# Performance work log

Hardware: AMD Instinct MI355X
Metric: run time of the kernel (lower is better)

## Reference

```python
import jax, jax.numpy as jnp
from jax import lax
import numpy as np

NS, NC = 12, 4            # n_state, n_ctrl
NSC = NS + NC             # tau = [x; u]
T, B = 50, 2048
U_LO, U_HI = -1.0, 1.0
LQR_ITERS = 3             # qp_iter-style outer LQR iterations
N_LS = 5                  # max_linesearch_iter
LS_DECAY = 0.5            # linesearch_decay


def setup_inputs() -> dict:
    key = jax.random.key(0)
    k0, k1, k2, k3, k4 = jax.random.split(key, 5)
    x0 = jax.random.normal(k0, (B, NS), jnp.float32)
    # PD quadratic cost: C = 0.1 * A A^T + I  (symmetric positive definite)
    A = jax.random.normal(k1, (T, B, NSC, NSC), jnp.float32) * (1.0 / np.sqrt(NSC))
    C = 0.1 * jnp.einsum('tbik,tbjk->tbij', A, A) + jnp.eye(NSC, dtype=jnp.float32)
    c = jax.random.normal(k2, (T, B, NSC), jnp.float32)
    # Near-identity stable linear dynamics x' = F [x;u] + f
    F = 0.02 * jax.random.normal(k3, (T, B, NS, NSC), jnp.float32)
    eye_pad = jnp.concatenate([0.98 * jnp.eye(NS, dtype=jnp.float32),
                               jnp.zeros((NS, NC), jnp.float32)], axis=-1)
    F = F + eye_pad
    f = 0.01 * jax.random.normal(k4, (T, B, NS), jnp.float32)
    return {'x0': x0, 'C': C, 'c': c, 'F': F, 'f': f}


def _riccati(C, c, F, f):
    """Backward Riccati recursion. Returns feedback gains K [T,B,NC,NS], k [T,B,NC]."""
    def step(carry, inp):
        V, v = carry                      # V: [B,NS,NS], v: [B,NS]
        Ct, ct, Ft, ft = inp
        FtV = jnp.einsum('bki,bkl->bil', Ft, V)          # F^T V: [B,NSC,NS]
        Q = Ct + jnp.einsum('bil,blj->bij', FtV, Ft)     # [B,NSC,NSC]
        q = ct + jnp.einsum('bki,bk->bi', Ft,
                            jnp.einsum('bij,bj->bi', V, ft) + v)
        Qxx, Qxu = Q[:, :NS, :NS], Q[:, :NS, NS:]
        Qux, Quu = Q[:, NS:, :NS], Q[:, NS:, NS:]
        qx, qu = q[:, :NS], q[:, NS:]
        rhs = jnp.concatenate([Qux, qu[:, :, None]], axis=-1)  # [B,NC,NS+1]
        sol = jnp.linalg.solve(Quu, rhs)
        K = -sol[:, :, :NS]               # [B,NC,NS]
        kk = -sol[:, :, NS]               # [B,NC]
        QxuK = jnp.einsum('bij,bjk->bik', Qxu, K)
        V_new = Qxx + QxuK + QxuK.transpose(0, 2, 1) \
            + jnp.einsum('bji,bjl,blk->bik', K, Quu, K)
        V_new = 0.5 * (V_new + V_new.transpose(0, 2, 1))
        v_new = qx + jnp.einsum('bij,bj->bi', Qxu, kk) \
            + jnp.einsum('bji,bj->bi', K, qu + jnp.einsum('bij,bj->bi', Quu, kk))
        return (V_new, v_new), (K, kk)

    Vz = jnp.zeros((C.shape[1], NS, NS), C.dtype)
    vz = jnp.zeros((C.shape[1], NS), C.dtype)
    _, (K, kk) = lax.scan(step, (Vz, vz), (C, c, F, f), reverse=True)
    return K, kk


def _rollout(alpha, x0, u_nom, K, kk, C, c, F, f):
    """Forward pass with box-clamped controls and line-search blending."""
    def step(carry, inp):
        x, cost = carry
        Ct, ct, Ft, ft, Kt, kt, unomt = inp
        u_lqr = jnp.einsum('bij,bj->bi', Kt, x) + kt
        u = jnp.clip((1.0 - alpha) * unomt + alpha * u_lqr, U_LO, U_HI)
        tau = jnp.concatenate([x, u], axis=-1)            # [B,NSC]
        cost = cost + 0.5 * jnp.einsum('bi,bij,bj->b', tau, Ct, tau) \
            + jnp.einsum('bi,bi->b', ct, tau)
        x_next = jnp.einsum('bij,bj->bi', Ft, tau) + ft
        return (x_next, cost), tau

    init = (x0, jnp.zeros(x0.shape[0], x0.dtype))
    (_, cost), taus = lax.scan(step, init, (C, c, F, f, K, kk, u_nom))
    return cost, taus  # cost [B], taus [T,B,NSC]


def reference(x0, C, c, F, f):
    alphas = LS_DECAY ** jnp.arange(N_LS, dtype=C.dtype)  # [N_LS]
    u_nom = jnp.zeros((T, x0.shape[0], NC), x0.dtype)
    taus = None
    for _ in range(LQR_ITERS):
        K, kk = _riccati(C, c, F, f)
        costs, taus_all = jax.vmap(
            lambda a: _rollout(a, x0, u_nom, K, kk, C, c, F, f))(alphas)
        # costs: [N_LS,B]; taus_all: [N_LS,T,B,NSC]. Pick best alpha per batch elem.
        best = jnp.argmin(costs, axis=0)                  # [B]
        taus = jnp.take_along_axis(taus_all,
                                   best[None, None, :, None], axis=0)[0]
        u_nom = taus[:, :, NS:]
    return taus  # [T, B, NSC] optimized trajectory [x; u]
```

## Files before the change

### kernel.cpp

```cpp
#include <hip/hip_runtime.h>
#include <math.h>

#define T_   50
#define B_   2048
#define NS_  12
#define NC_  4
#define NSC_ 16
#define LDC  20
#define TAUS_STRIDE 808

__device__ __forceinline__ float dot4f(const float4 a, const float4 b) {
    return a.x*b.x + a.y*b.y + a.z*b.z + a.w*b.w;
}
__device__ __forceinline__ void axpy4(float4& acc, float s, const float4 v) {
    acc.x += s*v.x; acc.y += s*v.y; acc.z += s*v.z; acc.w += s*v.w;
}

__device__ __forceinline__ void wsync() {
    __builtin_amdgcn_wave_barrier();
    __builtin_amdgcn_s_waitcnt(0xC07F);
    __builtin_amdgcn_wave_barrier();
}

__device__ __forceinline__ void bsync() {
    __builtin_amdgcn_wave_barrier();
    __builtin_amdgcn_s_waitcnt(0xC07F);
    __builtin_amdgcn_s_barrier();
    __builtin_amdgcn_wave_barrier();
}

struct RicPref { float4 rC, rAux; };

__device__ __forceinline__ RicPref ric_load(
    const float* Cg, const float* cg, const float* Fg, const float* fg,
    int t, int b, int lane)
{
    RicPref p;
    const size_t base = (size_t)t * B_ + b;
    p.rC = ((const float4*)(Cg + base*256))[lane];
    if (lane < 48)      p.rAux = ((const float4*)(Fg + base*192))[lane];
    else if (lane < 52) p.rAux = ((const float4*)(cg + base*16))[lane-48];
    else if (lane < 55) p.rAux = ((const float4*)(fg + base*12))[lane-52];
    return p;
}

__global__ __launch_bounds__(64) void riccati_kernel(
    const float* __restrict__ Cg, const float* __restrict__ cg,
    const float* __restrict__ Fg, const float* __restrict__ fg,
    float* __restrict__ Kk)
{
    const int b    = blockIdx.x;
    const int lane = threadIdx.x;

    __shared__ __align__(16) float sV[144];
    __shared__ __align__(16) float sv[12];
    __shared__ __align__(16) float sF[12*LDC];
    __shared__ __align__(16) float sC[16*LDC];
    __shared__ __align__(16) float sc[16];
    __shared__ __align__(16) float sf[12];
    __shared__ __align__(16) float sP[12*LDC];
    __shared__ __align__(16) float sQ[16*LDC];
    __shared__ __align__(16) float sq[16];
    __shared__ __align__(16) float stmp[12];
    __shared__ __align__(16) float sK[48];
    __shared__ __align__(16) float skk[4];
    __shared__ __align__(16) float sM[144];

    for (int i = lane; i < 144; i += 64) sV[i] = 0.f;
    if (lane < 12) sv[lane] = 0.f;

    RicPref cur = ric_load(Cg, cg, Fg, fg, T_-1, b, lane);
    wsync();

    for (int t = T_ - 1; t >= 0; --t) {
        const size_t base = (size_t)t * B_ + b;

        wsync();
        {
            const int row = lane >> 2, ch = (lane & 3) << 2;
            *(float4*)(sC + row*LDC + ch) = cur.rC;
            if (lane < 48)      *(float4*)(sF + row*LDC + ch) = cur.rAux;
            else if (lane < 52) ((float4*)sc)[lane-48] = cur.rAux;
            else if (lane < 55) ((float4*)sf)[lane-52] = cur.rAux;
        }
        RicPref nxt = ric_load(Cg, cg, Fg, fg, (t > 0) ? t-1 : 0, b, lane);
        wsync();

        if (lane < 48) {
            const int k = lane >> 2, jc = (lane & 3) << 2;
            float4 acc = make_float4(0.f,0.f,0.f,0.f);
            #pragma unroll
            for (int l = 0; l < 12; ++l) {
                axpy4(acc, sV[k*12 + l], *(const float4*)(sF + l*LDC + jc));
            }
            *(float4*)(sP + k*LDC + jc) = acc;
        } else if (lane < 60) {
            const int k = lane - 48;
            float acc = sv[k];
            #pragma unroll
            for (int l = 0; l < 12; ++l) acc += sV[k*12 + l] * sf[l];
            stmp[k] = acc;
        }
        wsync();

        {
            const int i = lane >> 2, jc = (lane & 3) << 2;
            float4 acc = *(const float4*)(sC + i*LDC + jc);
            #pragma unroll
            for (int k = 0; k < 12; ++k) {
                axpy4(acc, sF[k*LDC + i], *(const float4*)(sP + k*LDC + jc));
            }
            *(float4*)(sQ + i*LDC + jc) = acc;
        }
        if (lane < 16) {
            float acc = sc[lane];
            #pragma unroll
            for (int k = 0; k < 12; ++k) acc += sF[k*LDC + lane] * stmp[k];
            sq[lane] = acc;
        }
        wsync();

        {
            const float* Qu = sQ + 12*LDC + 12;
            const float a00=Qu[0],      a01=Qu[1],      a02=Qu[2],      a03=Qu[3];
            const float a11=Qu[LDC+1],  a12=Qu[LDC+2],  a13=Qu[LDC+3];
            const float a22=Qu[2*LDC+2],a23=Qu[2*LDC+3],a33=Qu[3*LDC+3];
            const float l00 = sqrtf(a00), i00 = 1.f/l00;
            const float l10 = a01*i00, l20 = a02*i00, l30 = a03*i00;
            const float l11 = sqrtf(a11 - l10*l10), i11 = 1.f/l11;
            const float l21 = (a12 - l20*l10)*i11;
            const float l31 = (a13 - l30*l10)*i11;
            const float l22 = sqrtf(a22 - l20*l20 - l21*l21), i22 = 1.f/l22;
            const float l32 = (a23 - l30*l20 - l31*l21)*i22;
            const float l33 = sqrtf(a33 - l30*l30 - l31*l31 - l32*l32), i33 = 1.f/l33;
            if (lane < 13) {
                float r0, r1, r2, r3;
                if (lane < 12) {
                    r0 = sQ[12*LDC + lane]; r1 = sQ[13*LDC + lane];
                    r2 = sQ[14*LDC + lane]; r3 = sQ[15*LDC + lane];
                } else {
                    r0 = sq[12]; r1 = sq[13]; r2 = sq[14]; r3 = sq[15];
                }
                const float y0 = r0*i00;
                const float y1 = (r1 - l10*y0)*i11;
                const float y2 = (r2 - l20*y0 - l21*y1)*i22;
                const float y3 = (r3 - l30*y0 - l31*y1 - l32*y2)*i33;
                const float z3 = y3*i33;
                const float z2 = (y2 - l32*z3)*i22;
                const float z1 = (y1 - l21*z2 - l31*z3)*i11;
                const float z0 = (y0 - l10*z1 - l20*z2 - l30*z3)*i00;
                if (lane < 12) {
                    sK[0*12+lane] = -z0; sK[1*12+lane] = -z1;
                    sK[2*12+lane] = -z2; sK[3*12+lane] = -z3;
                } else {
                    skk[0] = -z0; skk[1] = -z1; skk[2] = -z2; skk[3] = -z3;
                }
            }
        }
        wsync();

        if (lane < 52) {
            (Kk + base*52)[lane] = (lane < 48) ? sK[lane] : skk[lane-48];
        }
        if (lane < 36) {
            const int i = lane / 3, jc = (lane % 3) << 2;
            float4 acc = make_float4(0.f,0.f,0.f,0.f);
            #pragma unroll
            for (int m = 0; m < 4; ++m) {
                axpy4(acc, sK[m*12 + i], *(const float4*)(sQ + (12+m)*LDC + jc));
            }
            *(float4*)(sM + i*12 + jc) = acc;
        } else if (lane < 48) {
            const int i = lane - 36;
            float acc = sq[i];
            #pragma unroll
            for (int m = 0; m < 4; ++m) acc += sQ[i*LDC + 12 + m] * skk[m];
            sv[i] = acc;
        }
        wsync();

        if (lane < 36) {
            const int i = lane / 3, jc = (lane % 3) << 2;
            const float4 q  = *(const float4*)(sQ + i*LDC + jc);
            const float4 m1 = *(const float4*)(sM + i*12 + jc);
            const float t0 = sM[(jc+0)*12 + i];
            const float t1 = sM[(jc+1)*12 + i];
            const float t2 = sM[(jc+2)*12 + i];
            const float t3 = sM[(jc+3)*12 + i];
            float4 r;
            r.x = q.x + 0.5f*(m1.x + t0);
            r.y = q.y + 0.5f*(m1.y + t1);
            r.z = q.z + 0.5f*(m1.z + t2);
            r.w = q.w + 0.5f*(m1.w + t3);
            *(float4*)(sV + i*12 + jc) = r;
        }
        cur = nxt;
    }
}

struct RollAux { float4 r1, r2; };

__device__ __forceinline__ RollAux aux_load(
    const float* cg, const float* Fg, const float* fg, const float* Kk,
    int t, int b, int lane)
{
    RollAux p;
    const size_t base = (size_t)t * B_ + b;
    if (lane < 48)      p.r1 = ((const float4*)(Fg + base*192))[lane];
    else if (lane < 61) p.r1 = ((const float4*)(Kk + base*52))[lane-48];
    else                p.r1 = ((const float4*)(cg + base*16))[lane-61];
    if (lane == 0)      p.r2 = ((const float4*)(cg + base*16))[3];
    else if (lane < 4)  p.r2 = ((const float4*)(fg + base*12))[lane-1];
    return p;
}

__global__ __launch_bounds__(128, 4) void rollout_kernel(
    const float* __restrict__ x0g, const float* __restrict__ Cg,
    const float* __restrict__ cg,  const float* __restrict__ Fg,
    const float* __restrict__ fg,  const float* __restrict__ Kk,
    float* __restrict__ outg)
{
    const int b    = blockIdx.x;
    const int tid  = threadIdx.x;
    const int wave = tid >> 6;
    const int lane = tid & 63;

    __shared__ __align__(16) float staus[5*TAUS_STRIDE];
    __shared__ __align__(16) float sunom[T_*NC_];
    __shared__ __align__(16) float sx0[12];
    __shared__ __align__(16) float sC[16*LDC];
    __shared__ __align__(16) float sF[12*LDC];
    __shared__ __align__(16) float sKk[56];
    __shared__ __align__(16) float sc[16];
    __shared__ __align__(16) float sf[12];
    __shared__ float scost[5];
    __shared__ int   sbest;

    const int  task    = wave*64 + lane;
    const bool is_cost = task < 80;
    int a1, i1;
    if (is_cost) { a1 = task >> 4; i1 = task & 15; }
    else { const int v = task - 80; a1 = v / 12; i1 = v - a1*12; }
    const float* row1  = (is_cost ? (const float*)sC : (const float*)sF) + i1*LDC;
    const float* add1  = (is_cost ? (const float*)sc : (const float*)sf) + i1;
    float*       taub1 = staus + a1*TAUS_STRIDE;

    const int    iT    = (lane < 12) ? lane : 0;
    const float* rowT  = sF + iT*LDC;
    float*       taubT = staus + 4*TAUS_STRIDE;

    const int    aA  = (lane < 20) ? (lane >> 2) : 0;
    const int    iA  = lane & 3;
    const float  alA = ldexpf(1.0f, -aA);
    const float* KrA = sKk + iA*12;
    float*       tauA = staus + aA*TAUS_STRIDE;

    for (int i = tid; i < T_*NC_; i += 128) sunom[i] = 0.f;
    if (tid < 3) ((float4*)sx0)[tid] = ((const float4*)(x0g + (size_t)b*12))[tid];

    float4  curC;
    RollAux curA;
    if (wave == 0) curC = ((const float4*)(Cg + (size_t)b*256))[lane];
    else           curA = aux_load(cg, Fg, fg, Kk, 0, b, lane);
    bsync();

    for (int iter = 0; iter < 3; ++iter) {
        if (tid < 15) {
            const int a = tid / 3, ch = (tid % 3) << 2;
            *(float4*)(staus + a*TAUS_STRIDE + ch) = *(const float4*)(sx0 + ch);
        }
        float ca = 0.f;
        int toff = 0;

        for (int t = 0; t < T_; ++t) {
            bsync();
            if (wave == 0) {
                const int row = lane >> 2, ch = (lane & 3) << 2;
                *(float4*)(sC + row*LDC + ch) = curC;
                curC = ((const float4*)(Cg +
                          ((size_t)((t+1 < T_) ? t+1 : 0) * B_ + b)*256))[lane];
            } else {
                {
                    const int row = lane >> 2, ch = (lane & 3) << 2;
                    if (lane < 48)      *(float4*)(sF + row*LDC + ch) = curA.r1;
                    else if (lane < 61) ((float4*)sKk)[lane-48] = curA.r1;
                    else                ((float4*)sc)[lane-61]  = curA.r1;
                    if (lane == 0)      ((float4*)sc)[3] = curA.r2;
                    else if (lane < 4)  ((float4*)sf)[lane-1] = curA.r2;
                }
                curA = aux_load(cg, Fg, fg, Kk, (t+1 < T_) ? t+1 : 0, b, lane);
                wsync();
                if (lane < 20) {
                    const float* x = tauA + toff;
                    float ulqr = dot4f(*(const float4*)(KrA+0), *(const float4*)(x+0))
                               + dot4f(*(const float4*)(KrA+4), *(const float4*)(x+4))
                               + dot4f(*(const float4*)(KrA+8), *(const float4*)(x+8))
                               + sKk[48 + iA];
                    float u = (1.f - alA)*sunom[t*4 + iA] + alA*ulqr;
                    u = fminf(1.f, fmaxf(-1.f, u));
                    tauA[toff + 12 + iA] = u;
                }
            }
            bsync();

            const bool tnl = (t != T_-1);
            {
                const float* tau = taub1 + toff;
                const float  av  = add1[0];
                float acc = is_cost ? 0.f : av;
                acc += dot4f(*(const float4*)(row1+ 0), *(const float4*)(tau+ 0));
                acc += dot4f(*(const float4*)(row1+ 4), *(const float4*)(tau+ 4));
                acc += dot4f(*(const float4*)(row1+ 8), *(const float4*)(tau+ 8));
                acc += dot4f(*(const float4*)(row1+12), *(const float4*)(tau+12));
                if (is_cost)  ca += (0.5f*acc + av) * tau[i1];
                else if (tnl) taub1[toff + 16 + i1] = acc;
            }
            if (wave == 0 && lane < 12 && tnl) {
                const float* tau = taubT + toff;
                float acc = sf[iT];
                acc += dot4f(*(const float4*)(rowT+ 0), *(const float4*)(tau+ 0));
                acc += dot4f(*(const float4*)(rowT+ 4), *(const float4*)(tau+ 4));
                acc += dot4f(*(const float4*)(rowT+ 8), *(const float4*)(tau+ 8));
                acc += dot4f(*(const float4*)(rowT+12), *(const float4*)(tau+12));
                taubT[toff + 16 + iT] = acc;
            }
            toff += 16;
        }

        #pragma unroll
        for (int off = 1; off < 16; off <<= 1) ca += __shfl_xor(ca, off, 16);
        if (wave == 0) { if ((lane & 15) == 0) scost[lane >> 4] = ca; }
        else if (lane == 0) scost[4] = ca;
        bsync();
        if (tid == 0) {
            int bi = 0; float bc = scost[0];
            #pragma unroll
            for (int a = 1; a < 5; ++a) {
                if (scost[a] < bc) { bc = scost[a]; bi = a; }
            }
            sbest = bi;
        }
        bsync();
        const int best = sbest;

        for (int idx = tid; idx < T_*NC_; idx += 128) {
            const int tt = idx >> 2, i = idx & 3;
            sunom[idx] = staus[best*TAUS_STRIDE + tt*16 + 12 + i];
        }
        if (iter == 2) {
            for (int idx = tid; idx < T_*NSC_; idx += 128) {
                const int tt = idx >> 4, j = idx & 15;
                outg[((size_t)tt*B_ + b)*16 + j] = staus[best*TAUS_STRIDE + tt*16 + j];
            }
        }
        bsync();
    }
}

extern "C" void kernel_launch(void* const* d_in, const int* in_sizes, int n_in,
                              void* d_out, int out_size, void* d_ws, size_t ws_size,
                              hipStream_t stream) {
    const float* x0 = (const float*)d_in[0];
    const float* C  = (const float*)d_in[1];
    const float* c  = (const float*)d_in[2];
    const float* F  = (const float*)d_in[3];
    const float* f  = (const float*)d_in[4];
    float* out = (float*)d_out;
    float* Kk  = (float*)d_ws;

    riccati_kernel<<<B_, 64, 0, stream>>>(C, c, F, f, Kk);
    rollout_kernel<<<B_, 128, 0, stream>>>(x0, C, c, F, f, Kk, out);
}
```

Baseline: 443.8 us.

## Double-buffer rollout stage data and compute controls redundantly per wave to halve barriers

```diff
diff --git a/kernel.cpp b/kernel.cpp
--- a/kernel.cpp
+++ b/kernel.cpp
@@ -7,7 +7,7 @@
 #define NC_  4
 #define NSC_ 16
 #define LDC  20
-#define TAUS_STRIDE 808
+#define TS   804
 
 __device__ __forceinline__ float dot4f(const float4 a, const float4 b) {
     return a.x*b.x + a.y*b.y + a.z*b.z + a.w*b.w;
@@ -15,6 +15,7 @@
 __device__ __forceinline__ void axpy4(float4& acc, float s, const float4 v) {
     acc.x += s*v.x; acc.y += s*v.y; acc.z += s*v.z; acc.w += s*v.w;
 }
+__device__ __forceinline__ float4 ld4(const float* p) { return *(const float4*)p; }
 
 __device__ __forceinline__ void wsync() {
     __builtin_amdgcn_wave_barrier();
@@ -214,7 +215,7 @@
     return p;
 }
 
-__global__ __launch_bounds__(128, 4) void rollout_kernel(
+__global__ __launch_bounds__(128) void rollout_kernel(
     const float* __restrict__ x0g, const float* __restrict__ Cg,
     const float* __restrict__ cg,  const float* __restrict__ Fg,
     const float* __restrict__ fg,  const float* __restrict__ Kk,
@@ -225,14 +226,14 @@
     const int wave = tid >> 6;
     const int lane = tid & 63;
 
-    __shared__ __align__(16) float staus[5*TAUS_STRIDE];
+    __shared__ __align__(16) float staus[5*TS];
     __shared__ __align__(16) float sunom[T_*NC_];
     __shared__ __align__(16) float sx0[12];
-    __shared__ __align__(16) float sC[16*LDC];
-    __shared__ __align__(16) float sF[12*LDC];
-    __shared__ __align__(16) float sKk[56];
-    __shared__ __align__(16) float sc[16];
-    __shared__ __align__(16) float sf[12];
+    __shared__ __align__(16) float bC[2][16*LDC];
+    __shared__ __align__(16) float bF[2][12*LDC];
+    __shared__ __align__(16) float bK[2][56];
+    __shared__ __align__(16) float bcv[2][16];
+    __shared__ __align__(16) float bfv[2][12];
     __shared__ float scost[5];
     __shared__ int   sbest;
 
@@ -241,90 +242,116 @@
     int a1, i1;
     if (is_cost) { a1 = task >> 4; i1 = task & 15; }
     else { const int v = task - 80; a1 = v / 12; i1 = v - a1*12; }
-    const float* row1  = (is_cost ? (const float*)sC : (const float*)sF) + i1*LDC;
-    const float* add1  = (is_cost ? (const float*)sc : (const float*)sf) + i1;
-    float*       taub1 = staus + a1*TAUS_STRIDE;
-
-    const int    iT    = (lane < 12) ? lane : 0;
-    const float* rowT  = sF + iT*LDC;
-    float*       taubT = staus + 4*TAUS_STRIDE;
-
-    const int    aA  = (lane < 20) ? (lane >> 2) : 0;
-    const int    iA  = lane & 3;
-    const float  alA = ldexpf(1.0f, -aA);
-    const float* KrA = sKk + iA*12;
-    float*       tauA = staus + aA*TAUS_STRIDE;
+    float* taub1 = staus + a1*TS;
+    float* taub4 = staus + 4*TS;
+
+    const float* rowE = (is_cost ? bC[0] : bF[0]) + i1*LDC;
+    const float* rowO = (is_cost ? bC[1] : bF[1]) + i1*LDC;
+    const float* addE = (is_cost ? bcv[0] : bfv[0]) + i1;
+    const float* addO = (is_cost ? bcv[1] : bfv[1]) + i1;
+
+    const int   aU  = lane >> 2, jU = lane & 3;
+    const float alU = ldexpf(1.0f, -aU);
+
+    float4  rC;
+    RollAux rA;
+
+    auto stage = [&](float* bCn, float* bFn, float* bKn, float* bcn, float* bfn,
+                     int tn_next) {
+        const int row = lane >> 2, ch = (lane & 3) << 2;
+        *(float4*)(bCn + row*LDC + ch) = rC;
+        if (lane < 48)      *(float4*)(bFn + row*LDC + ch) = rA.r1;
+        else if (lane < 61) ((float4*)bKn)[lane-48] = rA.r1;
+        else                ((float4*)bcn)[lane-61] = rA.r1;
+        if (lane == 0)      ((float4*)bcn)[3] = rA.r2;
+        else if (lane < 4)  ((float4*)bfn)[lane-1] = rA.r2;
+        rC = ((const float4*)(Cg + ((size_t)tn_next * B_ + b)*256))[lane];
+        rA = aux_load(cg, Fg, fg, Kk, tn_next, b, lane);
+    };
+
+    auto step = [&](int t,
+                    const float* bKp, const float* bfp,
+                    float* bCn, float* bFn, float* bKn, float* bcn, float* bfn,
+                    const float* row1, const float* add1, float& ca) {
+        const int toff = t*16;
+
+        float uval = 0.f;
+        if (lane < 20) {
+            const float* Kr = bKp + jU*12;
+            const float* xU = staus + aU*TS + toff;
+            float ulqr = dot4f(ld4(Kr  ), ld4(xU  ))
+                       + dot4f(ld4(Kr+4), ld4(xU+4))
+                       + dot4f(ld4(Kr+8), ld4(xU+8))
+                       + bKp[48 + jU];
+            float u = (1.f - alU)*sunom[t*4 + jU] + alU*ulqr;
+            uval = fminf(1.f, fmaxf(-1.f, u));
+            if (wave == 0) staus[aU*TS + toff + 12 + jU] = uval;
+        }
+        float4 ul;
+        ul.x = __shfl(uval, a1*4 + 0, 64);
+        ul.y = __shfl(uval, a1*4 + 1, 64);
+        ul.z = __shfl(uval, a1*4 + 2, 64);
+        ul.w = __shfl(uval, a1*4 + 3, 64);
+
+        const float* xp = taub1 + toff;
+        const float4 x0 = ld4(xp), x1 = ld4(xp+4), x2 = ld4(xp+8);
+        const float  av = add1[0];
+        float acc = is_cost ? 0.f : av;
+        acc += dot4f(ld4(row1   ), x0);
+        acc += dot4f(ld4(row1+ 4), x1);
+        acc += dot4f(ld4(row1+ 8), x2);
+        acc += dot4f(ld4(row1+12), ul);
+        const bool tnl = (t != T_-1);
+        if (is_cost) {
+            float taui;
+            if (i1 < 12) taui = xp[i1];
+            else taui = (i1 == 12) ? ul.x : (i1 == 13) ? ul.y
+                      : (i1 == 14) ? ul.z : ul.w;
+            ca += (0.5f*acc + av) * taui;
+        } else if (tnl) {
+            taub1[toff + 16 + i1] = acc;
+        }
+
+        if (wave == 1 && lane < 12 && tnl) {
+            const float* Fr = (bCn == bC[1] ? bF[0] : bF[1]) + lane*LDC;
+            float acc4 = bfp[lane];
+            acc4 += dot4f(ld4(Fr   ), x0);
+            acc4 += dot4f(ld4(Fr+ 4), x1);
+            acc4 += dot4f(ld4(Fr+ 8), x2);
+            acc4 += dot4f(ld4(Fr+12), ul);
+            taub4[toff + 16 + lane] = acc4;
+        }
+
+        if (wave == 0) {
+            int tn = t + 2; if (tn >= T_) tn -= T_;
+            stage(bCn, bFn, bKn, bcn, bfn, tn);
+        }
+    };
 
     for (int i = tid; i < T_*NC_; i += 128) sunom[i] = 0.f;
     if (tid < 3) ((float4*)sx0)[tid] = ((const float4*)(x0g + (size_t)b*12))[tid];
 
-    float4  curC;
-    RollAux curA;
-    if (wave == 0) curC = ((const float4*)(Cg + (size_t)b*256))[lane];
-    else           curA = aux_load(cg, Fg, fg, Kk, 0, b, lane);
+    if (wave == 0) {
+        rC = ((const float4*)(Cg + (size_t)b*256))[lane];
+        rA = aux_load(cg, Fg, fg, Kk, 0, b, lane);
+        stage(bC[0], bF[0], bK[0], bcv[0], bfv[0], 1);
+    }
     bsync();
 
     for (int iter = 0; iter < 3; ++iter) {
         if (tid < 15) {
             const int a = tid / 3, ch = (tid % 3) << 2;
-            *(float4*)(staus + a*TAUS_STRIDE + ch) = *(const float4*)(sx0 + ch);
+            *(float4*)(staus + a*TS + ch) = *(const float4*)(sx0 + ch);
         }
         float ca = 0.f;
-        int toff = 0;
-
-        for (int t = 0; t < T_; ++t) {
+
+        for (int t = 0; t < T_; t += 2) {
             bsync();
-            if (wave == 0) {
-                const int row = lane >> 2, ch = (lane & 3) << 2;
-                *(float4*)(sC + row*LDC + ch) = curC;
-                curC = ((const float4*)(Cg +
-                          ((size_t)((t+1 < T_) ? t+1 : 0) * B_ + b)*256))[lane];
-            } else {
-                {
-                    const int row = lane >> 2, ch = (lane & 3) << 2;
-                    if (lane < 48)      *(float4*)(sF + row*LDC + ch) = curA.r1;
-                    else if (lane < 61) ((float4*)sKk)[lane-48] = curA.r1;
-                    else                ((float4*)sc)[lane-61]  = curA.r1;
-                    if (lane == 0)      ((float4*)sc)[3] = curA.r2;
-                    else if (lane < 4)  ((float4*)sf)[lane-1] = curA.r2;
-                }
-                curA = aux_load(cg, Fg, fg, Kk, (t+1 < T_) ? t+1 : 0, b, lane);
-                wsync();
-                if (lane < 20) {
-                    const float* x = tauA + toff;
-                    float ulqr = dot4f(*(const float4*)(KrA+0), *(const float4*)(x+0))
-                               + dot4f(*(const float4*)(KrA+4), *(const float4*)(x+4))
-                               + dot4f(*(const float4*)(KrA+8), *(const float4*)(x+8))
-                               + sKk[48 + iA];
-                    float u = (1.f - alA)*sunom[t*4 + iA] + alA*ulqr;
-                    u = fminf(1.f, fmaxf(-1.f, u));
-                    tauA[toff + 12 + iA] = u;
-                }
-            }
+            step(t,   bK[0], bfv[0],
+                 bC[1], bF[1], bK[1], bcv[1], bfv[1], rowE, addE, ca);
             bsync();
-
-            const bool tnl = (t != T_-1);
-            {
-                const float* tau = taub1 + toff;
-                const float  av  = add1[0];
-                float acc = is_cost ? 0.f : av;
-                acc += dot4f(*(const float4*)(row1+ 0), *(const float4*)(tau+ 0));
-                acc += dot4f(*(const float4*)(row1+ 4), *(const float4*)(tau+ 4));
-                acc += dot4f(*(const float4*)(row1+ 8), *(const float4*)(tau+ 8));
-                acc += dot4f(*(const float4*)(row1+12), *(const float4*)(tau+12));
-                if (is_cost)  ca += (0.5f*acc + av) * tau[i1];
-                else if (tnl) taub1[toff + 16 + i1] = acc;
-            }
-            if (wave == 0 && lane < 12 && tnl) {
-                const float* tau = taubT + toff;
-                float acc = sf[iT];
-                acc += dot4f(*(const float4*)(rowT+ 0), *(const float4*)(tau+ 0));
-                acc += dot4f(*(const float4*)(rowT+ 4), *(const float4*)(tau+ 4));
-                acc += dot4f(*(const float4*)(rowT+ 8), *(const float4*)(tau+ 8));
-                acc += dot4f(*(const float4*)(rowT+12), *(const float4*)(tau+12));
-                taubT[toff + 16 + iT] = acc;
-            }
-            toff += 16;
+            step(t+1, bK[1], bfv[1],
+                 bC[0], bF[0], bK[0], bcv[0], bfv[0], rowO, addO, ca);
         }
 
         #pragma unroll
@@ -345,12 +372,12 @@
 
         for (int idx = tid; idx < T_*NC_; idx += 128) {
             const int tt = idx >> 2, i = idx & 3;
-            sunom[idx] = staus[best*TAUS_STRIDE + tt*16 + 12 + i];
+            sunom[idx] = staus[best*TS + tt*16 + 12 + i];
         }
         if (iter == 2) {
             for (int idx = tid; idx < T_*NSC_; idx += 128) {
                 const int tt = idx >> 4, j = idx & 15;
-                outg[((size_t)tt*B_ + b)*16 + j] = staus[best*TAUS_STRIDE + tt*16 + j];
+                outg[((size_t)tt*B_ + b)*16 + j] = staus[best*TS + tt*16 + j];
             }
         }
         bsync();
```

Measured after the change: 520.0 us. 1.17x slower.

## Fuse Riccati backward pass into rollout kernel with shared-memory aliasing

Applied to the files above, without the earlier changes.

```diff
diff --git a/kernel.cpp b/kernel.cpp
--- a/kernel.cpp
+++ b/kernel.cpp
@@ -26,6 +26,12 @@
     __builtin_amdgcn_wave_barrier();
     __builtin_amdgcn_s_waitcnt(0xC07F);
     __builtin_amdgcn_s_barrier();
+    __builtin_amdgcn_wave_barrier();
+}
+
+__device__ __forceinline__ void full_drain() {
+    __builtin_amdgcn_wave_barrier();
+    __builtin_amdgcn_s_waitcnt(0x0070);
     __builtin_amdgcn_wave_barrier();
 }
 
@@ -42,160 +48,6 @@
     else if (lane < 52) p.rAux = ((const float4*)(cg + base*16))[lane-48];
     else if (lane < 55) p.rAux = ((const float4*)(fg + base*12))[lane-52];
     return p;
-}
-
-__global__ __launch_bounds__(64) void riccati_kernel(
-    const float* __restrict__ Cg, const float* __restrict__ cg,
-    const float* __restrict__ Fg, const float* __restrict__ fg,
-    float* __restrict__ Kk)
-{
-    const int b    = blockIdx.x;
-    const int lane = threadIdx.x;
-
-    __shared__ __align__(16) float sV[144];
-    __shared__ __align__(16) float sv[12];
-    __shared__ __align__(16) float sF[12*LDC];
-    __shared__ __align__(16) float sC[16*LDC];
-    __shared__ __align__(16) float sc[16];
-    __shared__ __align__(16) float sf[12];
-    __shared__ __align__(16) float sP[12*LDC];
-    __shared__ __align__(16) float sQ[16*LDC];
-    __shared__ __align__(16) float sq[16];
-    __shared__ __align__(16) float stmp[12];
-    __shared__ __align__(16) float sK[48];
-    __shared__ __align__(16) float skk[4];
-    __shared__ __align__(16) float sM[144];
-
-    for (int i = lane; i < 144; i += 64) sV[i] = 0.f;
-    if (lane < 12) sv[lane] = 0.f;
-
-    RicPref cur = ric_load(Cg, cg, Fg, fg, T_-1, b, lane);
-    wsync();
-
-    for (int t = T_ - 1; t >= 0; --t) {
-        const size_t base = (size_t)t * B_ + b;
-
-        wsync();
-        {
-            const int row = lane >> 2, ch = (lane & 3) << 2;
-            *(float4*)(sC + row*LDC + ch) = cur.rC;
-            if (lane < 48)      *(float4*)(sF + row*LDC + ch) = cur.rAux;
-            else if (lane < 52) ((float4*)sc)[lane-48] = cur.rAux;
-            else if (lane < 55) ((float4*)sf)[lane-52] = cur.rAux;
-        }
-        RicPref nxt = ric_load(Cg, cg, Fg, fg, (t > 0) ? t-1 : 0, b, lane);
-        wsync();
-
-        if (lane < 48) {
-            const int k = lane >> 2, jc = (lane & 3) << 2;
-            float4 acc = make_float4(0.f,0.f,0.f,0.f);
-            #pragma unroll
-            for (int l = 0; l < 12; ++l) {
-                axpy4(acc, sV[k*12 + l], *(const float4*)(sF + l*LDC + jc));
-            }
-            *(float4*)(sP + k*LDC + jc) = acc;
-        } else if (lane < 60) {
-            const int k = lane - 48;
-            float acc = sv[k];
-            #pragma unroll
-            for (int l = 0; l < 12; ++l) acc += sV[k*12 + l] * sf[l];
-            stmp[k] = acc;
-        }
-        wsync();
-
-        {
-            const int i = lane >> 2, jc = (lane & 3) << 2;
-            float4 acc = *(const float4*)(sC + i*LDC + jc);
-            #pragma unroll
-            for (int k = 0; k < 12; ++k) {
-                axpy4(acc, sF[k*LDC + i], *(const float4*)(sP + k*LDC + jc));
-            }
-            *(float4*)(sQ + i*LDC + jc) = acc;
-        }
-        if (lane < 16) {
-            float acc = sc[lane];
-            #pragma unroll
-            for (int k = 0; k < 12; ++k) acc += sF[k*LDC + lane] * stmp[k];
-            sq[lane] = acc;
-        }
-        wsync();
-
-        {
-            const float* Qu = sQ + 12*LDC + 12;
-            const float a00=Qu[0],      a01=Qu[1],      a02=Qu[2],      a03=Qu[3];
-            const float a11=Qu[LDC+1],  a12=Qu[LDC+2],  a13=Qu[LDC+3];
-            const float a22=Qu[2*LDC+2],a23=Qu[2*LDC+3],a33=Qu[3*LDC+3];
-            const float l00 = sqrtf(a00), i00 = 1.f/l00;
-            const float l10 = a01*i00, l20 = a02*i00, l30 = a03*i00;
-            const float l11 = sqrtf(a11 - l10*l10), i11 = 1.f/l11;
-            const float l21 = (a12 - l20*l10)*i11;
-            const float l31 = (a13 - l30*l10)*i11;
-            const float l22 = sqrtf(a22 - l20*l20 - l21*l21), i22 = 1.f/l22;
-            const float l32 = (a23 - l30*l20 - l31*l21)*i22;
-            const float l33 = sqrtf(a33 - l30*l30 - l31*l31 - l32*l32), i33 = 1.f/l33;
-            if (lane < 13) {
-                float r0, r1, r2, r3;
-                if (lane < 12) {
-                    r0 = sQ[12*LDC + lane]; r1 = sQ[13*LDC + lane];
-                    r2 = sQ[14*LDC + lane]; r3 = sQ[15*LDC + lane];
-                } else {
-                    r0 = sq[12]; r1 = sq[13]; r2 = sq[14]; r3 = sq[15];
-                }
-                const float y0 = r0*i00;
-                const float y1 = (r1 - l10*y0)*i11;
-                const float y2 = (r2 - l20*y0 - l21*y1)*i22;
-                const float y3 = (r3 - l30*y0 - l31*y1 - l32*y2)*i33;
-                const float z3 = y3*i33;
-                const float z2 = (y2 - l32*z3)*i22;
-                const float z1 = (y1 - l21*z2 - l31*z3)*i11;
-                const float z0 = (y0 - l10*z1 - l20*z2 - l30*z3)*i00;
-                if (lane < 12) {
-                    sK[0*12+lane] = -z0; sK[1*12+lane] = -z1;
-                    sK[2*12+lane] = -z2; sK[3*12+lane] = -z3;
-                } else {
-                    skk[0] = -z0; skk[1] = -z1; skk[2] = -z2; skk[3] = -z3;
-                }
-            }
-        }
-        wsync();
-
-        if (lane < 52) {
-            (Kk + base*52)[lane] = (lane < 48) ? sK[lane] : skk[lane-48];
-        }
-        if (lane < 36) {
-            const int i = lane / 3, jc = (lane % 3) << 2;
-            float4 acc = make_float4(0.f,0.f,0.f,0.f);
-            #pragma unroll
-            for (int m = 0; m < 4; ++m) {
-                axpy4(acc, sK[m*12 + i], *(const float4*)(sQ + (12+m)*LDC + jc));
-            }
-            *(float4*)(sM + i*12 + jc) = acc;
-        } else if (lane < 48) {
-            const int i = lane - 36;
-            float acc = sq[i];
-            #pragma unroll
-            for (int m = 0; m < 4; ++m) acc += sQ[i*LDC + 12 + m] * skk[m];
-            sv[i] = acc;
-        }
-        wsync();
-
-        if (lane < 36) {
-            const int i = lane / 3, jc = (lane % 3) << 2;
-            const float4 q  = *(const float4*)(sQ + i*LDC + jc);
-            const float4 m1 = *(const float4*)(sM + i*12 + jc);
-            const float t0 = sM[(jc+0)*12 + i];
-            const float t1 = sM[(jc+1)*12 + i];
-            const float t2 = sM[(jc+2)*12 + i];
-            const float t3 = sM[(jc+3)*12 + i];
-            float4 r;
-            r.x = q.x + 0.5f*(m1.x + t0);
-            r.y = q.y + 0.5f*(m1.y + t1);
-            r.z = q.z + 0.5f*(m1.z + t2);
-            r.w = q.w + 0.5f*(m1.w + t3);
-            *(float4*)(sV + i*12 + jc) = r;
-        }
-        cur = nxt;
-    }
 }
 
 struct RollAux { float4 r1, r2; };
@@ -214,10 +66,10 @@
     return p;
 }
 
-__global__ __launch_bounds__(128, 4) void rollout_kernel(
+__global__ __launch_bounds__(128, 4) void mpc_fused_kernel(
     const float* __restrict__ x0g, const float* __restrict__ Cg,
     const float* __restrict__ cg,  const float* __restrict__ Fg,
-    const float* __restrict__ fg,  const float* __restrict__ Kk,
+    const float* __restrict__ fg,  float* __restrict__ Kk,
     float* __restrict__ outg)
 {
     const int b    = blockIdx.x;
@@ -225,28 +77,182 @@
     const int wave = tid >> 6;
     const int lane = tid & 63;
 
-    __shared__ __align__(16) float staus[5*TAUS_STRIDE];
+    __shared__ __align__(16) float smem[5*TAUS_STRIDE];
     __shared__ __align__(16) float sunom[T_*NC_];
     __shared__ __align__(16) float sx0[12];
-    __shared__ __align__(16) float sC[16*LDC];
-    __shared__ __align__(16) float sF[12*LDC];
+    __shared__ __align__(16) float sC2[16*LDC];
+    __shared__ __align__(16) float sF2[12*LDC];
     __shared__ __align__(16) float sKk[56];
-    __shared__ __align__(16) float sc[16];
-    __shared__ __align__(16) float sf[12];
+    __shared__ __align__(16) float sc2[16];
+    __shared__ __align__(16) float sf2[12];
     __shared__ float scost[5];
     __shared__ int   sbest;
+
+    if (wave == 0) {
+        float* sV   = smem + 0;
+        float* sv   = smem + 160;
+        float* sF   = smem + 176;
+        float* sC   = smem + 416;
+        float* sc   = smem + 736;
+        float* sf   = smem + 752;
+        float* sP   = smem + 768;
+        float* sQ   = smem + 1008;
+        float* sq   = smem + 1328;
+        float* stmp = smem + 1344;
+        float* sK   = smem + 1360;
+        float* skk  = smem + 1408;
+        float* sM   = smem + 1424;
+
+        for (int i = lane; i < 144; i += 64) sV[i] = 0.f;
+        if (lane < 12) sv[lane] = 0.f;
+
+        RicPref cur = ric_load(Cg, cg, Fg, fg, T_-1, b, lane);
+        wsync();
+
+        for (int t = T_ - 1; t >= 0; --t) {
+            const size_t base = (size_t)t * B_ + b;
+
+            wsync();
+            {
+                const int row = lane >> 2, ch = (lane & 3) << 2;
+                *(float4*)(sC + row*LDC + ch) = cur.rC;
+                if (lane < 48)      *(float4*)(sF + row*LDC + ch) = cur.rAux;
+                else if (lane < 52) ((float4*)sc)[lane-48] = cur.rAux;
+                else if (lane < 55) ((float4*)sf)[lane-52] = cur.rAux;
+            }
+            RicPref nxt = ric_load(Cg, cg, Fg, fg, (t > 0) ? t-1 : 0, b, lane);
+            wsync();
+
+            if (lane < 48) {
+                const int k = lane >> 2, jc = (lane & 3) << 2;
+                float4 acc = make_float4(0.f,0.f,0.f,0.f);
+                #pragma unroll
+                for (int l = 0; l < 12; ++l) {
+                    axpy4(acc, sV[k*12 + l], *(const float4*)(sF + l*LDC + jc));
+                }
+                *(float4*)(sP + k*LDC + jc) = acc;
+            } else if (lane < 60) {
+                const int k = lane - 48;
+                float acc = sv[k];
+                #pragma unroll
+                for (int l = 0; l < 12; ++l) acc += sV[k*12 + l] * sf[l];
+                stmp[k] = acc;
+            }
+            wsync();
+
+            {
+                const int i = lane >> 2, jc = (lane & 3) << 2;
+                float4 acc = *(const float4*)(sC + i*LDC + jc);
+                #pragma unroll
+                for (int k = 0; k < 12; ++k) {
+                    axpy4(acc, sF[k*LDC + i], *(const float4*)(sP + k*LDC + jc));
+                }
+                *(float4*)(sQ + i*LDC + jc) = acc;
+            }
+            if (lane < 16) {
+                float acc = sc[lane];
+                #pragma unroll
+                for (int k = 0; k < 12; ++k) acc += sF[k*LDC + lane] * stmp[k];
+                sq[lane] = acc;
+            }
+            wsync();
+
+            {
+                const float* Qu = sQ + 12*LDC + 12;
+                const float a00=Qu[0],      a01=Qu[1],      a02=Qu[2],      a03=Qu[3];
+                const float a11=Qu[LDC+1],  a12=Qu[LDC+2],  a13=Qu[LDC+3];
+                const float a22=Qu[2*LDC+2],a23=Qu[2*LDC+3],a33=Qu[3*LDC+3];
+                const float l00 = sqrtf(a00), i00 = 1.f/l00;
+                const float l10 = a01*i00, l20 = a02*i00, l30 = a03*i00;
+                const float l11 = sqrtf(a11 - l10*l10), i11 = 1.f/l11;
+                const float l21 = (a12 - l20*l10)*i11;
+                const float l31 = (a13 - l30*l10)*i11;
+                const float l22 = sqrtf(a22 - l20*l20 - l21*l21), i22 = 1.f/l22;
+                const float l32 = (a23 - l30*l20 - l31*l21)*i22;
+                const float l33 = sqrtf(a33 - l30*l30 - l31*l31 - l32*l32), i33 = 1.f/l33;
+                if (lane < 13) {
+                    float r0, r1, r2, r3;
+                    if (lane < 12) {
+                        r0 = sQ[12*LDC + lane]; r1 = sQ[13*LDC + lane];
+                        r2 = sQ[14*LDC + lane]; r3 = sQ[15*LDC + lane];
+                    } else {
+                        r0 = sq[12]; r1 = sq[13]; r2 = sq[14]; r3 = sq[15];
+                    }
+                    const float y0 = r0*i00;
+                    const float y1 = (r1 - l10*y0)*i11;
+                    const float y2 = (r2 - l20*y0 - l21*y1)*i22;
+                    const float y3 = (r3 - l30*y0 - l31*y1 - l32*y2)*i33;
+                    const float z3 = y3*i33;
+                    const float z2 = (y2 - l32*z3)*i22;
+                    const float z1 = (y1 - l21*z2 - l31*z3)*i11;
+                    const float z0 = (y0 - l10*z1 - l20*z2 - l30*z3)*i00;
+                    if (lane < 12) {
+                        sK[0*12+lane] = -z0; sK[1*12+lane] = -z1;
+                        sK[2*12+lane] = -z2; sK[3*12+lane] = -z3;
+                    } else {
+                        skk[0] = -z0; skk[1] = -z1; skk[2] = -z2; skk[3] = -z3;
+                    }
+                }
+            }
+            wsync();
+
+            if (lane < 52) {
+                (Kk + base*52)[lane] = (lane < 48) ? sK[lane] : skk[lane-48];
+            }
+            if (lane < 36) {
+                const int i = lane / 3, jc = (lane % 3) << 2;
+                float4 acc = make_float4(0.f,0.f,0.f,0.f);
+                #pragma unroll
+                for (int m = 0; m < 4; ++m) {
+                    axpy4(acc, sK[m*12 + i], *(const float4*)(sQ + (12+m)*LDC + jc));
+                }
+                *(float4*)(sM + i*12 + jc) = acc;
+            } else if (lane < 48) {
+                const int i = lane - 36;
+                float acc = sq[i];
+                #pragma unroll
+                for (int m = 0; m < 4; ++m) acc += sQ[i*LDC + 12 + m] * skk[m];
+                sv[i] = acc;
+            }
+            wsync();
+
+            if (lane < 36) {
+                const int i = lane / 3, jc = (lane % 3) << 2;
+                const float4 q  = *(const float4*)(sQ + i*LDC + jc);
+                const float4 m1 = *(const float4*)(sM + i*12 + jc);
+                const float t0 = sM[(jc+0)*12 + i];
+                const float t1 = sM[(jc+1)*12 + i];
+                const float t2 = sM[(jc+2)*12 + i];
+                const float t3 = sM[(jc+3)*12 + i];
+                float4 r;
+                r.x = q.x + 0.5f*(m1.x + t0);
+                r.y = q.y + 0.5f*(m1.y + t1);
+                r.z = q.z + 0.5f*(m1.z + t2);
+                r.w = q.w + 0.5f*(m1.w + t3);
+                *(float4*)(sV + i*12 + jc) = r;
+            }
+            cur = nxt;
+        }
+        full_drain();
+    } else {
+        for (int i = lane; i < T_*NC_; i += 64) sunom[i] = 0.f;
+        if (lane < 3) ((float4*)sx0)[lane] = ((const float4*)(x0g + (size_t)b*12))[lane];
+    }
+    bsync();
+
+    float* staus = smem;
 
     const int  task    = wave*64 + lane;
     const bool is_cost = task < 80;
     int a1, i1;
     if (is_cost) { a1 = task >> 4; i1 = task & 15; }
     else { const int v = task - 80; a1 = v / 12; i1 = v - a1*12; }
-    const float* row1  = (is_cost ? (const float*)sC : (const float*)sF) + i1*LDC;
-    const float* add1  = (is_cost ? (const float*)sc : (const float*)sf) + i1;
+    const float* row1  = (is_cost ? (const float*)sC2 : (const float*)sF2) + i1*LDC;
+    const float* add1  = (is_cost ? (const float*)sc2 : (const float*)sf2) + i1;
     float*       taub1 = staus + a1*TAUS_STRIDE;
 
     const int    iT    = (lane < 12) ? lane : 0;
-    const float* rowT  = sF + iT*LDC;
+    const float* rowT  = sF2 + iT*LDC;
     float*       taubT = staus + 4*TAUS_STRIDE;
 
     const int    aA  = (lane < 20) ? (lane >> 2) : 0;
@@ -255,9 +261,6 @@
     const float* KrA = sKk + iA*12;
     float*       tauA = staus + aA*TAUS_STRIDE;
 
-    for (int i = tid; i < T_*NC_; i += 128) sunom[i] = 0.f;
-    if (tid < 3) ((float4*)sx0)[tid] = ((const float4*)(x0g + (size_t)b*12))[tid];
-
     float4  curC;
     RollAux curA;
     if (wave == 0) curC = ((const float4*)(Cg + (size_t)b*256))[lane];
@@ -276,17 +279,17 @@
             bsync();
             if (wave == 0) {
                 const int row = lane >> 2, ch = (lane & 3) << 2;
-                *(float4*)(sC + row*LDC + ch) = curC;
+                *(float4*)(sC2 + row*LDC + ch) = curC;
                 curC = ((const float4*)(Cg +
                           ((size_t)((t+1 < T_) ? t+1 : 0) * B_ + b)*256))[lane];
             } else {
                 {
                     const int row = lane >> 2, ch = (lane & 3) << 2;
-                    if (lane < 48)      *(float4*)(sF + row*LDC + ch) = curA.r1;
+                    if (lane < 48)      *(float4*)(sF2 + row*LDC + ch) = curA.r1;
                     else if (lane < 61) ((float4*)sKk)[lane-48] = curA.r1;
-                    else                ((float4*)sc)[lane-61]  = curA.r1;
-                    if (lane == 0)      ((float4*)sc)[3] = curA.r2;
-                    else if (lane < 4)  ((float4*)sf)[lane-1] = curA.r2;
+                    else                ((float4*)sc2)[lane-61]  = curA.r1;
+                    if (lane == 0)      ((float4*)sc2)[3] = curA.r2;
+                    else if (lane < 4)  ((float4*)sf2)[lane-1] = curA.r2;
                 }
                 curA = aux_load(cg, Fg, fg, Kk, (t+1 < T_) ? t+1 : 0, b, lane);
                 wsync();
@@ -317,7 +320,7 @@
             }
             if (wave == 0 && lane < 12 && tnl) {
                 const float* tau = taubT + toff;
-                float acc = sf[iT];
+                float acc = sf2[iT];
                 acc += dot4f(*(const float4*)(rowT+ 0), *(const float4*)(tau+ 0));
                 acc += dot4f(*(const float4*)(rowT+ 4), *(const float4*)(tau+ 4));
                 acc += dot4f(*(const float4*)(rowT+ 8), *(const float4*)(tau+ 8));
@@ -368,6 +371,5 @@
     float* out = (float*)d_out;
     float* Kk  = (float*)d_ws;
 
-    riccati_kernel<<<B_, 64, 0, stream>>>(C, c, F, f, Kk);
-    rollout_kernel<<<B_, 128, 0, stream>>>(x0, C, c, F, f, Kk, out);
-}
+    mpc_fused_kernel<<<B_, 128, 0, stream>>>(x0, C, c, F, f, Kk, out);
+}
```

After: 499.0 us. +12.4%, slower.
